# Kernel optimization log

Measured on AMD Instinct MI355X. Metric: run time of the kernel, lower is better.

## Reference

```python
import jax, jax.numpy as jnp
import numpy as np

B, L, D, NLAYERS, KCONV = 8, 2048, 1024, 3, 4


def setup_inputs() -> dict:
    key = jax.random.key(0)
    ks = jax.random.split(key, 8)
    inp = {
        "x": jax.random.normal(ks[0], (B, L, D), jnp.float32),
        "conv_w": jax.random.normal(ks[1], (NLAYERS, D, KCONV), jnp.float32) * 0.02,
        "conv_b": jnp.zeros((NLAYERS, D), jnp.float32),
        "wr_w": jax.random.normal(ks[2], (NLAYERS, D, D), jnp.float32) * (1.0 / np.sqrt(D)),
        "wr_b": jnp.zeros((NLAYERS, D), jnp.float32),
        "wi_w": jax.random.normal(ks[3], (NLAYERS, D, D), jnp.float32) * (1.0 / np.sqrt(D)),
        "wi_b": jnp.zeros((NLAYERS, D), jnp.float32),
        "log_a": 3.0 + 0.1 * jax.random.normal(ks[4], (NLAYERS, D), jnp.float32),
        "wo_w": jax.random.normal(ks[5], (NLAYERS, D, D), jnp.float32) * (1.0 / np.sqrt(D)),
        "norm_w": jnp.ones((NLAYERS, D), jnp.float32),
        "norm_out_w": jnp.ones((D,), jnp.float32),
    }
    return inp


def _rmsnorm(x, w, eps=1e-6):
    return x * w * jax.lax.rsqrt(jnp.mean(x * x, axis=-1, keepdims=True) + eps)


def _parallel_scan(a, b):
    # h_t = a_t * h_{t-1} + b_t  via log-space prefix scan (h0 = 0)
    a32 = a.astype(jnp.float32)
    b32 = b.astype(jnp.float32)
    log_A = jnp.cumsum(jnp.log(jnp.maximum(a32, 1e-7)), axis=1)
    log_A = jnp.maximum(log_A, -80.0)  # a<=1 so log_A<=0 already
    A = jnp.exp(log_A)
    h = A * jnp.cumsum(b32 * jnp.exp(-log_A), axis=1)
    return h.astype(a.dtype)


def _rglru_layer(x, cw, cb, wrw, wrb, wiw, wib, la, wow, nw):
    # causal depthwise conv1d, kernel 4, left pad 3
    Lx = x.shape[1]
    xp = jnp.pad(x, ((0, 0), (KCONV - 1, 0), (0, 0)))
    x_conv = cb + sum(xp[:, k:k + Lx, :] * cw[:, k] for k in range(KCONV))
    r_t = jax.nn.sigmoid(x_conv @ wrw.T + wrb)
    i_t = jax.nn.sigmoid(x_conv @ wiw.T + wib)
    a_base = jax.nn.sigmoid(la.astype(jnp.float32)).astype(x.dtype)
    a_t = a_base ** (8.0 * r_t)
    b_t = jnp.sqrt(jnp.clip(1.0 - a_t * a_t, 1e-6, None)) * (i_t * x_conv)
    h = _parallel_scan(a_t, b_t)
    return _rmsnorm(h @ wow.T, nw)


def reference(x, conv_w, conv_b, wr_w, wr_b, wi_w, wi_b, log_a, wo_w, norm_w, norm_out_w):
    h = x
    for l in range(NLAYERS):
        h = _rglru_layer(h, conv_w[l], conv_b[l], wr_w[l], wr_b[l],
                         wi_w[l], wi_b[l], log_a[l], wo_w[l], norm_w[l])
    return _rmsnorm(h, norm_out_w)
```

## Files before the change

### kernel.cpp

```cpp
#include <hip/hip_runtime.h>
#include <type_traits>

#define BDIM 8
#define LDIM 2048
#define DDIM 1024
#define NL 3
#define K4 4
#define MDIM (BDIM * LDIM)
#define BK32 32
#define NT32 (DDIM / BK32)

typedef __bf16 bf16x8 __attribute__((ext_vector_type(8)));
typedef __bf16 bf16x4 __attribute__((ext_vector_type(4)));
typedef float f32x4 __attribute__((ext_vector_type(4)));
typedef const __attribute__((address_space(1))) void gvoid_t;
typedef __attribute__((address_space(3))) void svoid_t;

__device__ __forceinline__ void load16(const void* g, void* lds_uniform) {
    __builtin_amdgcn_global_load_lds((gvoid_t*)g, (svoid_t*)lds_uniform, 16, 0, 0);
}

#define SBAR()                                  \
    do {                                        \
        asm volatile("" ::: "memory");          \
        __builtin_amdgcn_s_barrier();           \
        asm volatile("" ::: "memory");          \
    } while (0)
#define WAITV(N) asm volatile("s_waitcnt vmcnt(" #N ")" ::: "memory")
#define LGKM0() asm volatile("s_waitcnt lgkmcnt(0)" ::: "memory")
#define SCHED0() __builtin_amdgcn_sched_barrier(0)

__device__ __forceinline__ unsigned lds_addr(const void* p) {
    return (unsigned)(unsigned long long)(svoid_t*)(p);
}
__device__ __forceinline__ bf16x8 dsr16(unsigned a) {
    f32x4 r;
    asm volatile("ds_read_b128 %0, %1" : "=v"(r) : "v"(a));
    return __builtin_bit_cast(bf16x8, r);
}

__global__ void cvt_bf16(const float* __restrict__ s, __bf16* __restrict__ d, int n) {
    int i = blockIdx.x * 256 + threadIdx.x;
    if (i < n) d[i] = (__bf16)s[i];
}

__global__ __launch_bounds__(256) void cvt_interleave(const float* __restrict__ wr,
                                                      const float* __restrict__ wi,
                                                      __bf16* __restrict__ w2, int n) {
    int i = blockIdx.x * 256 + threadIdx.x;
    if (i >= n) return;
    int k = i & (DDIM - 1);
    int ld = i >> 10;
    int l = ld >> 10;
    int d = ld & (DDIM - 1);
    size_t base = ((size_t)l * 2 * DDIM + 2 * d) * DDIM + k;
    w2[base] = (__bf16)wr[i];
    w2[base + DDIM] = (__bf16)wi[i];
}

template <typename T>
__global__ __launch_bounds__(256) void conv_kernel(const T* __restrict__ X,
                                                   const float* __restrict__ cw,
                                                   const float* __restrict__ cb,
                                                   __bf16* __restrict__ XC) {
    int idx = blockIdx.x * 256 + threadIdx.x;
    int d = (idx & (DDIM / 4 - 1)) << 2;
    int t = (idx >> 8) & (LDIM - 1);
    int b = idx >> 19;
    float wv[4][4];
    *(float4*)wv[0] = ((const float4*)cw)[d + 0];
    *(float4*)wv[1] = ((const float4*)cw)[d + 1];
    *(float4*)wv[2] = ((const float4*)cw)[d + 2];
    *(float4*)wv[3] = ((const float4*)cw)[d + 3];
    float4 cbv = *(const float4*)(cb + d);
    float acc[4] = {cbv.x, cbv.y, cbv.z, cbv.w};
#pragma unroll
    for (int k = 0; k < K4; k++) {
        int tt = t + k - (K4 - 1);
        if (tt >= 0) {
            size_t off = ((size_t)(b * LDIM + tt) << 10) + d;
            float xv[4];
            if constexpr (std::is_same<T, float>::value) {
                float4 v = *(const float4*)(X + off);
                xv[0] = v.x; xv[1] = v.y; xv[2] = v.z; xv[3] = v.w;
            } else {
                bf16x4 v = *(const bf16x4*)(X + off);
                xv[0] = (float)v.x; xv[1] = (float)v.y; xv[2] = (float)v.z; xv[3] = (float)v.w;
            }
#pragma unroll
            for (int j = 0; j < 4; j++) acc[j] += xv[j] * wv[j][k];
        }
    }
    bf16x4 o;
    o.x = (__bf16)acc[0]; o.y = (__bf16)acc[1]; o.z = (__bf16)acc[2]; o.w = (__bf16)acc[3];
    *(bf16x4*)(XC + ((size_t)(b * LDIM + t) << 10) + d) = o;
}

__global__ __launch_bounds__(512, 2) void gate_gemm(
    const __bf16* __restrict__ A, const __bf16* __restrict__ W2,
    const float* __restrict__ wrb, const float* __restrict__ wib,
    const float* __restrict__ la,
    __bf16* __restrict__ LOGA, __bf16* __restrict__ BB) {
    __shared__ __attribute__((aligned(16))) __bf16 sm[65536];
    int tid = threadIdx.x;
    int wave = tid >> 6, lane = tid & 63;
    int wm = wave >> 2, wn = wave & 3;
    int fr = lane & 15, quad = lane >> 4;

    int nx = gridDim.x;
    int bid = blockIdx.y * nx + blockIdx.x;
    int cpx = (nx * gridDim.y) >> 3;
    int sw = (bid & 7) * cpx + (bid >> 3);
    int bm0 = (sw / nx) * 256;
    int bn0 = (sw % nx) * 256;

    const __bf16* Ag = A + (size_t)bm0 * DDIM;
    const __bf16* Bg = W2 + (size_t)bn0 * DDIM;

    f32x4 acc[8][4];
    f32x4 zero = {0.f, 0.f, 0.f, 0.f};
#pragma unroll
    for (int i = 0; i < 8; i++)
#pragma unroll
        for (int j = 0; j < 4; j++) acc[i][j] = zero;

    unsigned smb = lds_addr(sm);
    unsigned adA[2][4], adB[4];
#pragma unroll
    for (int mh = 0; mh < 2; mh++)
#pragma unroll
        for (int mi = 0; mi < 4; mi++) {
            int row = wm * 128 + (mh * 4 + mi) * 16 + fr;
            adA[mh][mi] = smb + 2u * (row * 32 + ((quad ^ ((row >> 1) & 3)) << 3));
        }
#pragma unroll
    for (int ni = 0; ni < 4; ni++) {
        int row = wn * 64 + ni * 16 + fr;
        adB[ni] = smb + 2u * (8192 + row * 32 + ((quad ^ ((row >> 1) & 3)) << 3));
    }
    int r0 = tid >> 2, g0 = (tid & 3) ^ ((r0 >> 1) & 3);
    int r1 = (512 + tid) >> 2, g1 = ((512 + tid) & 3) ^ ((r1 >> 1) & 3);
    const __bf16* gA0 = Ag + (size_t)r0 * DDIM + g0 * 8;
    const __bf16* gA1 = Ag + (size_t)r1 * DDIM + g1 * 8;
    const __bf16* gB0 = Bg + (size_t)r0 * DDIM + g0 * 8;
    const __bf16* gB1 = Bg + (size_t)r1 * DDIM + g1 * 8;
    int lb0 = wave * 512, lb1 = 4096 + wave * 512;

    auto STAGE = [&](int buf, int t) {
        int lo = buf * 16384;
        load16(gA0 + t * BK32, sm + lo + lb0);
        load16(gA1 + t * BK32, sm + lo + lb1);
        load16(gB0 + t * BK32, sm + lo + 8192 + lb0);
        load16(gB1 + t * BK32, sm + lo + 8192 + lb1);
    };

    STAGE(0, 0);
    STAGE(1, 1);
    STAGE(2, 2);
    for (int t4 = 0; t4 < NT32; t4 += 4) {
#pragma unroll
        for (int tt = 0; tt < 4; tt++) {
            int t = t4 + tt;
            if (t + 2 < NT32) { WAITV(8); }
            else if (t + 1 < NT32) { WAITV(4); }
            else { WAITV(0); }
            SBAR();
            if (t + 3 < NT32) STAGE((tt + 3) & 3, t + 3);
            unsigned tb = (unsigned)(tt * 32768);
            bf16x8 bfm[4], af[4];
#pragma unroll
            for (int ni = 0; ni < 4; ni++) bfm[ni] = dsr16(adB[ni] + tb);
#pragma unroll
            for (int mi = 0; mi < 4; mi++) af[mi] = dsr16(adA[0][mi] + tb);
            LGKM0();
            SCHED0();
            __builtin_amdgcn_s_setprio(1);
#pragma unroll
            for (int ni = 0; ni < 4; ni++)
#pragma unroll
                for (int mi = 0; mi < 4; mi++)
                    acc[mi][ni] = __builtin_amdgcn_mfma_f32_16x16x32_bf16(
                        af[mi], bfm[ni], acc[mi][ni], 0, 0, 0);
            __builtin_amdgcn_s_setprio(0);
#pragma unroll
            for (int mi = 0; mi < 4; mi++) af[mi] = dsr16(adA[1][mi] + tb);
            LGKM0();
            SCHED0();
            __builtin_amdgcn_s_setprio(1);
#pragma unroll
            for (int ni = 0; ni < 4; ni++)
#pragma unroll
                for (int mi = 0; mi < 4; mi++)
                    acc[4 + mi][ni] = __builtin_amdgcn_mfma_f32_16x16x32_bf16(
                        af[mi], bfm[ni], acc[4 + mi][ni], 0, 0, 0);
            __builtin_amdgcn_s_setprio(0);
        }
    }

    float* Lt = (float*)&sm[0];
    int colg = (tid & 31) * 8;
    int d0 = (bn0 >> 1) + (colg >> 1);
    float rb[4], ibv[4], lnab[4];
    {
        float4 r4 = *(const float4*)(wrb + d0);
        float4 i4 = *(const float4*)(wib + d0);
        float4 l4 = *(const float4*)(la + d0);
        float lav[4] = {l4.x, l4.y, l4.z, l4.w};
        rb[0] = r4.x; rb[1] = r4.y; rb[2] = r4.z; rb[3] = r4.w;
        ibv[0] = i4.x; ibv[1] = i4.y; ibv[2] = i4.z; ibv[3] = i4.w;
#pragma unroll
        for (int j = 0; j < 4; j++) lnab[j] = __logf(1.f / (1.f + __expf(-lav[j])));
    }
#pragma unroll
    for (int mi = 0; mi < 8; mi++) {
        __syncthreads();
#pragma unroll
        for (int ni = 0; ni < 4; ni++) {
            int col = wn * 64 + ni * 16 + fr;
#pragma unroll
            for (int reg = 0; reg < 4; reg++)
                Lt[(wm * 16 + quad * 4 + reg) * 260 + col] = acc[mi][ni][reg];
        }
        __syncthreads();
#pragma unroll
        for (int hf = 0; hf < 2; hf++) {
            int r = (tid >> 5) + hf * 16;
            int m = bm0 + (r >> 4) * 128 + mi * 16 + (r & 15);
            float vv[8];
            *(f32x4*)&vv[0] = *(const f32x4*)&Lt[r * 260 + colg];
            *(f32x4*)&vv[4] = *(const f32x4*)&Lt[r * 260 + colg + 4];
            bf16x4 xcv = *(const bf16x4*)(A + (size_t)m * DDIM + d0);
            bf16x4 og, ob;
#pragma unroll
            for (int j = 0; j < 4; j++) {
                float rv = 1.f / (1.f + __expf(-(vv[2 * j] + rb[j])));
                float iv = 1.f / (1.f + __expf(-(vv[2 * j + 1] + ibv[j])));
                float lga = 8.f * rv * lnab[j];
                float a = __expf(lga);
                float bt = sqrtf(fmaxf(1.f - a * a, 1e-6f)) * (iv * (float)xcv[j]);
                og[j] = (__bf16)lga;
                ob[j] = (__bf16)bt;
            }
            *(bf16x4*)(LOGA + (size_t)m * DDIM + d0) = og;
            *(bf16x4*)(BB + (size_t)m * DDIM + d0) = ob;
        }
    }
}

__global__ __launch_bounds__(512, 2) void out_gemm(
    const __bf16* __restrict__ A, const __bf16* __restrict__ Wo, __bf16* __restrict__ HW) {
    __shared__ __attribute__((aligned(16))) __bf16 sm[65536];
    int tid = threadIdx.x;
    int wave = tid >> 6, lane = tid & 63;
    int wm = wave >> 2, wn = wave & 3;
    int fr = lane & 15, quad = lane >> 4;

    int nx = gridDim.x;
    int bid = blockIdx.y * nx + blockIdx.x;
    int cpx = (nx * gridDim.y) >> 3;
    int sw = (bid & 7) * cpx + (bid >> 3);
    int bm0 = (sw / nx) * 256;
    int bn0 = (sw % nx) * 256;

    const __bf16* Ag = A + (size_t)bm0 * DDIM;
    const __bf16* Bg = Wo + (size_t)bn0 * DDIM;

    f32x4 acc[8][4];
    f32x4 zero = {0.f, 0.f, 0.f, 0.f};
#pragma unroll
    for (int i = 0; i < 8; i++)
#pragma unroll
        for (int j = 0; j < 4; j++) acc[i][j] = zero;

    unsigned smb = lds_addr(sm);
    unsigned adA[2][4], adB[4];
#pragma unroll
    for (int mh = 0; mh < 2; mh++)
#pragma unroll
        for (int mi = 0; mi < 4; mi++) {
            int row = wm * 128 + (mh * 4 + mi) * 16 + fr;
            adA[mh][mi] = smb + 2u * (row * 32 + ((quad ^ ((row >> 1) & 3)) << 3));
        }
#pragma unroll
    for (int ni = 0; ni < 4; ni++) {
        int row = wn * 64 + ni * 16 + fr;
        adB[ni] = smb + 2u * (8192 + row * 32 + ((quad ^ ((row >> 1) & 3)) << 3));
    }
    int r0 = tid >> 2, g0 = (tid & 3) ^ ((r0 >> 1) & 3);
    int r1 = (512 + tid) >> 2, g1 = ((512 + tid) & 3) ^ ((r1 >> 1) & 3);
    const __bf16* gA0 = Ag + (size_t)r0 * DDIM + g0 * 8;
    const __bf16* gA1 = Ag + (size_t)r1 * DDIM + g1 * 8;
    const __bf16* gB0 = Bg + (size_t)r0 * DDIM + g0 * 8;
    const __bf16* gB1 = Bg + (size_t)r1 * DDIM + g1 * 8;
    int lb0 = wave * 512, lb1 = 4096 + wave * 512;

    auto STAGE = [&](int buf, int t) {
        int lo = buf * 16384;
        load16(gA0 + t * BK32, sm + lo + lb0);
        load16(gA1 + t * BK32, sm + lo + lb1);
        load16(gB0 + t * BK32, sm + lo + 8192 + lb0);
        load16(gB1 + t * BK32, sm + lo + 8192 + lb1);
    };

    STAGE(0, 0);
    STAGE(1, 1);
    STAGE(2, 2);
    for (int t4 = 0; t4 < NT32; t4 += 4) {
#pragma unroll
        for (int tt = 0; tt < 4; tt++) {
            int t = t4 + tt;
            if (t + 2 < NT32) { WAITV(8); }
            else if (t + 1 < NT32) { WAITV(4); }
            else { WAITV(0); }
            SBAR();
            if (t + 3 < NT32) STAGE((tt + 3) & 3, t + 3);
            unsigned tb = (unsigned)(tt * 32768);
            bf16x8 bfm[4], af[4];
#pragma unroll
            for (int ni = 0; ni < 4; ni++) bfm[ni] = dsr16(adB[ni] + tb);
#pragma unroll
            for (int mi = 0; mi < 4; mi++) af[mi] = dsr16(adA[0][mi] + tb);
            LGKM0();
            SCHED0();
            __builtin_amdgcn_s_setprio(1);
#pragma unroll
            for (int ni = 0; ni < 4; ni++)
#pragma unroll
                for (int mi = 0; mi < 4; mi++)
                    acc[mi][ni] = __builtin_amdgcn_mfma_f32_16x16x32_bf16(
                        af[mi], bfm[ni], acc[mi][ni], 0, 0, 0);
            __builtin_amdgcn_s_setprio(0);
#pragma unroll
            for (int mi = 0; mi < 4; mi++) af[mi] = dsr16(adA[1][mi] + tb);
            LGKM0();
            SCHED0();
            __builtin_amdgcn_s_setprio(1);
#pragma unroll
            for (int ni = 0; ni < 4; ni++)
#pragma unroll
                for (int mi = 0; mi < 4; mi++)
                    acc[4 + mi][ni] = __builtin_amdgcn_mfma_f32_16x16x32_bf16(
                        af[mi], bfm[ni], acc[4 + mi][ni], 0, 0, 0);
            __builtin_amdgcn_s_setprio(0);
        }
    }

    float* Lt = (float*)&sm[0];
    int colg = (tid & 31) * 8;
    int n0 = bn0 + colg;
#pragma unroll
    for (int mi = 0; mi < 8; mi++) {
        __syncthreads();
#pragma unroll
        for (int ni = 0; ni < 4; ni++) {
            int col = wn * 64 + ni * 16 + fr;
#pragma unroll
            for (int reg = 0; reg < 4; reg++)
                Lt[(wm * 16 + quad * 4 + reg) * 260 + col] = acc[mi][ni][reg];
        }
        __syncthreads();
#pragma unroll
        for (int hf = 0; hf < 2; hf++) {
            int r = (tid >> 5) + hf * 16;
            int m = bm0 + (r >> 4) * 128 + mi * 16 + (r & 15);
            float vv[8];
            *(f32x4*)&vv[0] = *(const f32x4*)&Lt[r * 260 + colg];
            *(f32x4*)&vv[4] = *(const f32x4*)&Lt[r * 260 + colg + 4];
            bf16x8 o;
#pragma unroll
            for (int j = 0; j < 8; j++) o[j] = (__bf16)vv[j];
            *(bf16x8*)(HW + (size_t)m * DDIM + n0) = o;
        }
    }
}

#define SCH 32
#define SCT 64
__global__ __launch_bounds__(1024) void scan_kernel(const __bf16* __restrict__ LOGA,
                                                    const __bf16* __restrict__ BB,
                                                    __bf16* __restrict__ H) {
    int b = blockIdx.y;
    int dl = threadIdx.x & 31;
    int d = blockIdx.x * 32 + dl;
    int c = threadIdx.x >> 5;
    size_t base = ((size_t)b * LDIM + (size_t)c * SCT) * DDIM + d;
    const __bf16* pga = LOGA + base;
    const __bf16* pbb = BB + base;
    __bf16* pH = H + base;

    float S = 0.f;
#pragma unroll 8
    for (int t = 0; t < SCT; t++) S += (float)pga[(size_t)t * DDIM];
    __shared__ float sS[SCH][32];
    sS[c][dl] = S;
    __syncthreads();
    float L0 = 0.f;
    for (int cc = 0; cc < c; cc++) L0 += sS[cc][dl];

    float Lr = L0, lcp = fmaxf(L0, -80.f), hB = 0.f;
#pragma unroll 4
    for (int t = 0; t < SCT; t++) {
        float lga = (float)pga[(size_t)t * DDIM];
        Lr += lga;
        float lc = fmaxf(Lr, -80.f);
        hB = __expf(lc - lcp) * hB + (float)pbb[(size_t)t * DDIM];
        lcp = lc;
    }
    float Ac = __expf(fmaxf(Lr, -80.f) - fmaxf(L0, -80.f));
    __shared__ float sA[SCH][32], sB[SCH][32];
    sA[c][dl] = Ac;
    sB[c][dl] = hB;
    __syncthreads();
    float hin = 0.f;
    for (int cc = 0; cc < c; cc++) hin = sA[cc][dl] * hin + sB[cc][dl];

    Lr = L0;
    lcp = fmaxf(L0, -80.f);
    float h = hin;
#pragma unroll 4
    for (int t = 0; t < SCT; t++) {
        float lga = (float)pga[(size_t)t * DDIM];
        Lr += lga;
        float lc = fmaxf(Lr, -80.f);
        h = __expf(lc - lcp) * h + (float)pbb[(size_t)t * DDIM];
        lcp = lc;
        pH[(size_t)t * DDIM] = (__bf16)h;
    }
}

template <typename TI, typename TO>
__global__ __launch_bounds__(256) void rmsnorm_kernel(const TI* __restrict__ X,
                                                      const float* __restrict__ w,
                                                      TO* __restrict__ Y) {
    int row = blockIdx.x;
    int tid = threadIdx.x;
    size_t off = (size_t)row * DDIM + tid * 4;
    float v[4];
    if constexpr (std::is_same<TI, float>::value) {
        float4 t = *(const float4*)(X + off);
        v[0] = t.x; v[1] = t.y; v[2] = t.z; v[3] = t.w;
    } else {
        bf16x4 t = *(const bf16x4*)(X + off);
        v[0] = (float)t.x; v[1] = (float)t.y; v[2] = (float)t.z; v[3] = (float)t.w;
    }
    float s = v[0] * v[0] + v[1] * v[1] + v[2] * v[2] + v[3] * v[3];
#pragma unroll
    for (int o = 32; o > 0; o >>= 1) s += __shfl_down(s, o);
    __shared__ float sw[4];
    if ((tid & 63) == 0) sw[tid >> 6] = s;
    __syncthreads();
    float tot = sw[0] + sw[1] + sw[2] + sw[3];
    float scale = rsqrtf(tot * (1.f / (float)DDIM) + 1e-6f);
    float4 wv = ((const float4*)w)[tid];
    float o0 = v[0] * wv.x * scale, o1 = v[1] * wv.y * scale;
    float o2 = v[2] * wv.z * scale, o3 = v[3] * wv.w * scale;
    if constexpr (std::is_same<TO, float>::value) {
        float4 o = {o0, o1, o2, o3};
        *(float4*)(Y + off) = o;
    } else {
        bf16x4 o;
        o.x = (__bf16)o0; o.y = (__bf16)o1; o.z = (__bf16)o2; o.w = (__bf16)o3;
        *(bf16x4*)(Y + off) = o;
    }
}

extern "C" void kernel_launch(void* const* d_in, const int* in_sizes, int n_in,
                              void* d_out, int out_size, void* d_ws, size_t ws_size,
                              hipStream_t stream) {
    const float* x = (const float*)d_in[0];
    const float* conv_w = (const float*)d_in[1];
    const float* conv_b = (const float*)d_in[2];
    const float* wr_w = (const float*)d_in[3];
    const float* wr_b = (const float*)d_in[4];
    const float* wi_w = (const float*)d_in[5];
    const float* wi_b = (const float*)d_in[6];
    const float* log_a = (const float*)d_in[7];
    const float* wo_w = (const float*)d_in[8];
    const float* norm_w = (const float*)d_in[9];
    const float* norm_out_w = (const float*)d_in[10];

    const size_t W2SZ = (size_t)NL * 2 * DDIM * DDIM;
    const size_t WOSZ = (size_t)NL * DDIM * DDIM;
    const size_t MD = (size_t)MDIM * DDIM;
    __bf16* w2 = (__bf16*)d_ws;
    __bf16* wo16 = w2 + W2SZ;
    __bf16* XC = wo16 + WOSZ;
    __bf16* LGA = XC + MD;
    __bf16* BBf = LGA + MD;
    __bf16* Hb = BBf + MD;
    __bf16* HWb = Hb + MD;
    __bf16* PNb = HWb + MD;

    int nw = (int)WOSZ;
    cvt_interleave<<<(nw + 255) / 256, 256, 0, stream>>>(wr_w, wi_w, w2, nw);
    cvt_bf16<<<(nw + 255) / 256, 256, 0, stream>>>(wo_w, wo16, nw);

    for (int l = 0; l < NL; l++) {
        if (l == 0)
            conv_kernel<float><<<(MDIM * (DDIM / 4)) / 256, 256, 0, stream>>>(
                x, conv_w, conv_b, XC);
        else
            conv_kernel<__bf16><<<(MDIM * (DDIM / 4)) / 256, 256, 0, stream>>>(
                PNb, conv_w + (size_t)l * DDIM * K4, conv_b + (size_t)l * DDIM, XC);
        gate_gemm<<<dim3(2 * DDIM / 256, MDIM / 256), 512, 0, stream>>>(
            XC, w2 + (size_t)l * 2 * DDIM * DDIM,
            wr_b + (size_t)l * DDIM, wi_b + (size_t)l * DDIM, log_a + (size_t)l * DDIM,
            LGA, BBf);
        scan_kernel<<<dim3(DDIM / 32, BDIM), 1024, 0, stream>>>(LGA, BBf, Hb);
        out_gemm<<<dim3(DDIM / 256, MDIM / 256), 512, 0, stream>>>(
            Hb, wo16 + (size_t)l * DDIM * DDIM, HWb);
        rmsnorm_kernel<__bf16, __bf16><<<MDIM, 256, 0, stream>>>(
            HWb, norm_w + (size_t)l * DDIM, PNb);
    }
    rmsnorm_kernel<__bf16, float><<<MDIM, 256, 0, stream>>>(PNb, norm_out_w, (float*)d_out);
}
```

Before: 912.1 us.

## Software-pipeline LDS fragment loads in GEMM loops and fuse final RMSNorms

```diff
diff --git a/kernel.cpp b/kernel.cpp
--- a/kernel.cpp
+++ b/kernel.cpp
@@ -157,42 +157,52 @@
     STAGE(0, 0);
     STAGE(1, 1);
     STAGE(2, 2);
+    WAITV(8);
+    SBAR();
+    bf16x8 bs[2][4], acur[4];
+#pragma unroll
+    for (int ni = 0; ni < 4; ni++) bs[0][ni] = dsr16(adB[ni]);
+#pragma unroll
+    for (int mi = 0; mi < 4; mi++) acur[mi] = dsr16(adA[0][mi]);
+
     for (int t4 = 0; t4 < NT32; t4 += 4) {
 #pragma unroll
-        for (int tt = 0; tt < 4; tt++) {
-            int t = t4 + tt;
-            if (t + 2 < NT32) { WAITV(8); }
-            else if (t + 1 < NT32) { WAITV(4); }
+        for (int u = 0; u < 4; u++) {
+            int t = t4 + u;
+            unsigned tb = (unsigned)(u * 32768);
+            LGKM0();
+            SCHED0();
+            bf16x8 af2[4];
+#pragma unroll
+            for (int mi = 0; mi < 4; mi++) af2[mi] = dsr16(adA[1][mi] + tb);
+            __builtin_amdgcn_s_setprio(1);
+#pragma unroll
+            for (int ni = 0; ni < 4; ni++)
+#pragma unroll
+                for (int mi = 0; mi < 4; mi++)
+                    acc[mi][ni] = __builtin_amdgcn_mfma_f32_16x16x32_bf16(
+                        acur[mi], bs[u & 1][ni], acc[mi][ni], 0, 0, 0);
+            __builtin_amdgcn_s_setprio(0);
+            LGKM0();
+            SCHED0();
+            if (t + 2 < NT32) { WAITV(4); }
             else { WAITV(0); }
             SBAR();
-            if (t + 3 < NT32) STAGE((tt + 3) & 3, t + 3);
-            unsigned tb = (unsigned)(tt * 32768);
-            bf16x8 bfm[4], af[4];
-#pragma unroll
-            for (int ni = 0; ni < 4; ni++) bfm[ni] = dsr16(adB[ni] + tb);
-#pragma unroll
-            for (int mi = 0; mi < 4; mi++) af[mi] = dsr16(adA[0][mi] + tb);
-            LGKM0();
-            SCHED0();
-            __builtin_amdgcn_s_setprio(1);
-#pragma unroll
-            for (int ni = 0; ni < 4; ni++)
-#pragma unroll
-                for (int mi = 0; mi < 4; mi++)
-                    acc[mi][ni] = __builtin_amdgcn_mfma_f32_16x16x32_bf16(
-                        af[mi], bfm[ni], acc[mi][ni], 0, 0, 0);
-            __builtin_amdgcn_s_setprio(0);
-#pragma unroll
-            for (int mi = 0; mi < 4; mi++) af[mi] = dsr16(adA[1][mi] + tb);
-            LGKM0();
-            SCHED0();
+            if (t + 3 < NT32) STAGE((u + 3) & 3, t + 3);
+            if (t + 1 < NT32) {
+                unsigned tb2 = (unsigned)(((u + 1) & 3) * 32768);
+#pragma unroll
+                for (int ni = 0; ni < 4; ni++) bs[(u + 1) & 1][ni] = dsr16(adB[ni] + tb2);
+#pragma unroll
+                for (int mi = 0; mi < 4; mi++) acur[mi] = dsr16(adA[0][mi] + tb2);
+            }
             __builtin_amdgcn_s_setprio(1);
 #pragma unroll
             for (int ni = 0; ni < 4; ni++)
 #pragma unroll
                 for (int mi = 0; mi < 4; mi++)
                     acc[4 + mi][ni] = __builtin_amdgcn_mfma_f32_16x16x32_bf16(
-                        af[mi], bfm[ni], acc[4 + mi][ni], 0, 0, 0);
+                        af2[mi], bs[u & 1][ni], acc[4 + mi][ni], 0, 0, 0);
             __builtin_amdgcn_s_setprio(0);
         }
     }
@@ -305,42 +315,52 @@
     STAGE(0, 0);
     STAGE(1, 1);
     STAGE(2, 2);
+    WAITV(8);
+    SBAR();
+    bf16x8 bs[2][4], acur[4];
+#pragma unroll
+    for (int ni = 0; ni < 4; ni++) bs[0][ni] = dsr16(adB[ni]);
+#pragma unroll
+    for (int mi = 0; mi < 4; mi++) acur[mi] = dsr16(adA[0][mi]);
+
     for (int t4 = 0; t4 < NT32; t4 += 4) {
 #pragma unroll
-        for (int tt = 0; tt < 4; tt++) {
-            int t = t4 + tt;
-            if (t + 2 < NT32) { WAITV(8); }
-            else if (t + 1 < NT32) { WAITV(4); }
+        for (int u = 0; u < 4; u++) {
+            int t = t4 + u;
+            unsigned tb = (unsigned)(u * 32768);
+            LGKM0();
+            SCHED0();
+            bf16x8 af2[4];
+#pragma unroll
+            for (int mi = 0; mi < 4; mi++) af2[mi] = dsr16(adA[1][mi] + tb);
+            __builtin_amdgcn_s_setprio(1);
+#pragma unroll
+            for (int ni = 0; ni < 4; ni++)
+#pragma unroll
+                for (int mi = 0; mi < 4; mi++)
+                    acc[mi][ni] = __builtin_amdgcn_mfma_f32_16x16x32_bf16(
+                        acur[mi], bs[u & 1][ni], acc[mi][ni], 0, 0, 0);
+            __builtin_amdgcn_s_setprio(0);
+            LGKM0();
+            SCHED0();
+            if (t + 2 < NT32) { WAITV(4); }
             else { WAITV(0); }
             SBAR();
-            if (t + 3 < NT32) STAGE((tt + 3) & 3, t + 3);
-            unsigned tb = (unsigned)(tt * 32768);
-            bf16x8 bfm[4], af[4];
-#pragma unroll
-            for (int ni = 0; ni < 4; ni++) bfm[ni] = dsr16(adB[ni] + tb);
-#pragma unroll
-            for (int mi = 0; mi < 4; mi++) af[mi] = dsr16(adA[0][mi] + tb);
-            LGKM0();
-            SCHED0();
-            __builtin_amdgcn_s_setprio(1);
-#pragma unroll
-            for (int ni = 0; ni < 4; ni++)
-#pragma unroll
-                for (int mi = 0; mi < 4; mi++)
-                    acc[mi][ni] = __builtin_amdgcn_mfma_f32_16x16x32_bf16(
-                        af[mi], bfm[ni], acc[mi][ni], 0, 0, 0);
-            __builtin_amdgcn_s_setprio(0);
-#pragma unroll
-            for (int mi = 0; mi < 4; mi++) af[mi] = dsr16(adA[1][mi] + tb);
-            LGKM0();
-            SCHED0();
+            if (t + 3 < NT32) STAGE((u + 3) & 3, t + 3);
+            if (t + 1 < NT32) {
+                unsigned tb2 = (unsigned)(((u + 1) & 3) * 32768);
+#pragma unroll
+                for (int ni = 0; ni < 4; ni++) bs[(u + 1) & 1][ni] = dsr16(adB[ni] + tb2);
+#pragma unroll
+                for (int mi = 0; mi < 4; mi++) acur[mi] = dsr16(adA[0][mi] + tb2);
+            }
             __builtin_amdgcn_s_setprio(1);
 #pragma unroll
             for (int ni = 0; ni < 4; ni++)
 #pragma unroll
                 for (int mi = 0; mi < 4; mi++)
                     acc[4 + mi][ni] = __builtin_amdgcn_mfma_f32_16x16x32_bf16(
-                        af[mi], bfm[ni], acc[4 + mi][ni], 0, 0, 0);
+                        af2[mi], bs[u & 1][ni], acc[4 + mi][ni], 0, 0, 0);
             __builtin_amdgcn_s_setprio(0);
         }
     }
@@ -464,6 +484,38 @@
     }
 }
 
+__global__ __launch_bounds__(256) void rmsnorm2_kernel(const __bf16* __restrict__ X,
+                                                       const float* __restrict__ w1,
+                                                       const float* __restrict__ w2,
+                                                       float* __restrict__ Y) {
+    int row = blockIdx.x;
+    int tid = threadIdx.x;
+    size_t off = (size_t)row * DDIM + tid * 4;
+    bf16x4 t = *(const bf16x4*)(X + off);
+    float v[4] = {(float)t.x, (float)t.y, (float)t.z, (float)t.w};
+    float s = v[0] * v[0] + v[1] * v[1] + v[2] * v[2] + v[3] * v[3];
+#pragma unroll
+    for (int o = 32; o > 0; o >>= 1) s += __shfl_down(s, o);
+    __shared__ float sw[8];
+    if ((tid & 63) == 0) sw[tid >> 6] = s;
+    __syncthreads();
+    float scale1 = rsqrtf((sw[0] + sw[1] + sw[2] + sw[3]) * (1.f / (float)DDIM) + 1e-6f);
+    float4 w1v = ((const float4*)w1)[tid];
+    float y[4] = {v[0] * w1v.x * scale1, v[1] * w1v.y * scale1,
+                  v[2] * w1v.z * scale1, v[3] * w1v.w * scale1};
+    float s2 = y[0] * y[0] + y[1] * y[1] + y[2] * y[2] + y[3] * y[3];
+#pragma unroll
+    for (int o = 32; o > 0; o >>= 1) s2 += __shfl_down(s2, o);
+    __syncthreads();
+    if ((tid & 63) == 0) sw[4 + (tid >> 6)] = s2;
+    __syncthreads();
+    float scale2 = rsqrtf((sw[4] + sw[5] + sw[6] + sw[7]) * (1.f / (float)DDIM) + 1e-6f);
+    float4 w2v = ((const float4*)w2)[tid];
+    float4 o = {y[0] * w2v.x * scale2, y[1] * w2v.y * scale2,
+                y[2] * w2v.z * scale2, y[3] * w2v.w * scale2};
+    *(float4*)(Y + off) = o;
+}
+
 extern "C" void kernel_launch(void* const* d_in, const int* in_sizes, int n_in,
                               void* d_out, int out_size, void* d_ws, size_t ws_size,
                               hipStream_t stream) {
@@ -509,8 +561,10 @@
         scan_kernel<<<dim3(DDIM / 32, BDIM), 1024, 0, stream>>>(LGA, BBf, Hb);
         out_gemm<<<dim3(DDIM / 256, MDIM / 256), 512, 0, stream>>>(
             Hb, wo16 + (size_t)l * DDIM * DDIM, HWb);
-        rmsnorm_kernel<__bf16, __bf16><<<MDIM, 256, 0, stream>>>(
-            HWb, norm_w + (size_t)l * DDIM, PNb);
-    }
-    rmsnorm_kernel<__bf16, float><<<MDIM, 256, 0, stream>>>(PNb, norm_out_w, (float*)d_out);
-}
+        if (l < NL - 1)
+            rmsnorm_kernel<__bf16, __bf16><<<MDIM, 256, 0, stream>>>(
+                HWb, norm_w + (size_t)l * DDIM, PNb);
+    }
+    rmsnorm2_kernel<<<MDIM, 256, 0, stream>>>(
+        HWb, norm_w + (size_t)(NL - 1) * DDIM, norm_out_w, (float*)d_out);
+}
```

After: 1.171 ms. 1.28x slower.
